# Kernel optimization log

Hardware: AMD Instinct MI355X
Metric: run time of the kernel (lower is better)

Reference implementation:

```python
import jax, jax.numpy as jnp
import numpy as np

U = 1024   # units
DK = 1024  # attention inner dim (dk)
B, T, D = 64, 128, 256


def setup_inputs() -> dict:
    key = jax.random.key(0)
    ks = jax.random.split(key, 20)
    s_w = 0.02   # dense-kernel init scale
    s_a = 0.03   # ~glorot for (1, dk) attention vectors
    inp = {
        'x': jax.random.normal(ks[0], (B, T, D), jnp.float32),
        'kernel': jax.random.normal(ks[1], (D, 5 * U), jnp.float32) * s_w,
        'recurrent_kernel': jax.random.normal(ks[2], (U, 5 * U), jnp.float32) * s_w,
        'cell_kernel': jax.random.normal(ks[3], (U, 5 * U), jnp.float32) * s_w,
        'bias': jnp.zeros((5 * U,), jnp.float32),
        'aggregation': jax.random.normal(ks[4], (3 * U, U), jnp.float32) * s_w,
    }
    att_names = ['up_att_downl', 'up_att_downr', 'up_att_randl', 'up_att_randr',
                 'rand_att_upl', 'rand_att_upr', 'rand_att_downl', 'rand_att_downr',
                 'down_att_upl', 'down_att_upr', 'down_att_randl', 'down_att_randr']
    for i, n in enumerate(att_names):
        inp[n] = jax.random.normal(ks[5 + i], (1, DK), jnp.float32) * s_a
    return inp


def _cumsoftmax_l2r(x):
    return jnp.cumsum(jax.nn.softmax(x, axis=-1), axis=-1)


def _cumsoftmax_r2l(x):
    # reverse, softmax+cumsum, reverse back (softmax is permutation-equivariant)
    return jnp.cumsum(jax.nn.softmax(x, axis=-1)[..., ::-1], axis=-1)[..., ::-1]


def _forward(x, kernel, recurrent_kernel, cell_kernel, bias, aggregation,
             up_att_downl, up_att_downr, up_att_randl, up_att_randr,
             rand_att_upl, rand_att_upr, rand_att_downl, rand_att_downr,
             down_att_upl, down_att_upr, down_att_randl, down_att_randr):
    # Rank-1 collapse of (v w_l)(u w_r)^T v chains: scalar = w_l . w_r
    s_ud = jnp.sum(up_att_downl * up_att_downr)
    s_ur = jnp.sum(up_att_randl * up_att_randr)
    s_ru = jnp.sum(rand_att_upl * rand_att_upr)
    s_rd = jnp.sum(rand_att_downl * rand_att_downr)
    s_du = jnp.sum(down_att_upl * down_att_upr)
    s_dr = jnp.sum(down_att_randl * down_att_randr)

    # precompute input projection for all timesteps: [T, B, 5U]
    xw = jnp.einsum('btd,dk->tbk', x, kernel) + bias

    def step(carry, xw_t):
        c, h = carry
        z = xw_t + h @ recurrent_kernel + c @ cell_kernel  # [B, 5U]
        up = _cumsoftmax_l2r(z[:, :U])
        down = _cumsoftmax_r2l(z[:, U:2 * U])
        rand = z[:, 2 * U:3 * U]
        du = jnp.sum(down * up, axis=-1, keepdims=True)    # <down, up> per batch
        ru = jnp.sum(rand * up, axis=-1, keepdims=True)
        dr = jnp.sum(down * rand, axis=-1, keepdims=True)
        O1 = jax.nn.sigmoid(s_ud * up * du) + jax.nn.sigmoid(s_ur * up * ru)
        O2 = jax.nn.sigmoid(s_ru * rand * ru) + jax.nn.sigmoid(s_rd * rand * dr)
        O3 = jax.nn.sigmoid(s_du * down * du) + jax.nn.sigmoid(s_dr * down * dr)
        f_gate = jax.nn.sigmoid(jnp.concatenate([O1, O2, O3], axis=-1) @ aggregation)
        i_gate = 1.0 - f_gate
        o_gate = z[:, 3 * U:4 * U]          # NOTE: no sigmoid in the original
        c_in = jnp.tanh(z[:, 4 * U:])
        c_new = f_gate * c + i_gate * c_in
        h_new = o_gate * jnp.tanh(c_new)
        return (c_new, h_new), h_new

    init = (jnp.zeros((x.shape[0], U), x.dtype), jnp.zeros((x.shape[0], U), x.dtype))
    _, hs = jax.lax.scan(step, init, xw)
    return jnp.transpose(hs, (1, 0, 2))  # return_sequences=True -> [B, T, U]


def reference(x, kernel, recurrent_kernel, cell_kernel, bias, aggregation,
              up_att_downl, up_att_downr, up_att_randl, up_att_randr,
              rand_att_upl, rand_att_upr, rand_att_downl, rand_att_downr,
              down_att_upl, down_att_upr, down_att_randl, down_att_randr):
    return _forward(x, kernel, recurrent_kernel, cell_kernel, bias, aggregation,
                    up_att_downl, up_att_downr, up_att_randl, up_att_randr,
                    rand_att_upl, rand_att_upr, rand_att_downl, rand_att_downr,
                    down_att_upl, down_att_upr, down_att_randl, down_att_randr)
```

## Files before the change

kernel.cpp:

```cpp
#include <hip/hip_runtime.h>
#include <hip/hip_bf16.h>


typedef short  bf16x8 __attribute__((ext_vector_type(8)));
typedef float  f32x4  __attribute__((ext_vector_type(4)));
typedef _Float16 f16;
typedef _Float16 f16x8 __attribute__((ext_vector_type(8)));
typedef __hip_bfloat16 bf16;
typedef unsigned long long u64;

#define U 1024
#define BATCH 64
#define TSTEPS 128
#define DIM 256
#define N5 5120
#define K2 2048

#define OFF_WRC   0u
#define OFF_KT    20971520u
#define OFF_AGGT  23592960u
#define OFF_XBF   29884416u
#define OFF_ZP    34078720u
#define OFF_ABUF  39321600u
#define OFF_C32   39845888u
#define OFF_OBUF  40108032u
#define OFF_SCAL  40501248u
#define OFF_CTR   40501504u
#define OFF_PB    OFF_KT

#define NBLK_A 160
#define NBLK_B 64
#define NBLK   224
#define FPAD   8

#define KT_OFF 131072

#define MFMA16(a,b,c)  __builtin_amdgcn_mfma_f32_16x16x32_bf16((a),(b),(c),0,0,0)
#define MFMA16H(a,b,c) __builtin_amdgcn_mfma_f32_16x16x32_f16((a),(b),(c),0,0,0)

__global__ __launch_bounds__(256) void k_xconv(const float* __restrict__ in,
                                               f16* __restrict__ o, int n4) {
    const int i = blockIdx.x * 256 + threadIdx.x;
    if (i < n4) {
        const float4 v = ((const float4*)in)[i];
        f16 tmp[4] = {(f16)v.x, (f16)v.y, (f16)v.z, (f16)v.w};
        ((uint2*)o)[i] = *(const uint2*)tmp;
    }
}

__global__ __launch_bounds__(256) void k_transpose_h(const float* __restrict__ in,
                                                     f16* __restrict__ out,
                                                     int C, int out_stride, int out_off) {
    __shared__ f16 tile[64][65];
    const int tc = blockIdx.x * 64, tr = blockIdx.y * 64;
    const int tx = threadIdx.x & 63, ty0 = threadIdx.x >> 6;
#pragma unroll
    for (int i = 0; i < 64; i += 4)
        tile[ty0 + i][tx] = (f16)(in[(tr + ty0 + i) * C + tc + tx]);
    __syncthreads();
#pragma unroll
    for (int i = 0; i < 64; i += 4)
        out[(tc + ty0 + i) * out_stride + out_off + tr + tx] = tile[tx][ty0 + i];
}

__global__ __launch_bounds__(256) void k_transpose_b(const float* __restrict__ in,
                                                     bf16* __restrict__ out,
                                                     int C, int out_stride, int out_off) {
    __shared__ bf16 tile[64][65];
    const int tc = blockIdx.x * 64, tr = blockIdx.y * 64;
    const int tx = threadIdx.x & 63, ty0 = threadIdx.x >> 6;
#pragma unroll
    for (int i = 0; i < 64; i += 4)
        tile[ty0 + i][tx] = __float2bfloat16(in[(tr + ty0 + i) * C + tc + tx]);
    __syncthreads();
#pragma unroll
    for (int i = 0; i < 64; i += 4)
        out[(tc + ty0 + i) * out_stride + out_off + tr + tx] = tile[tx][ty0 + i];
}

struct AttPtrs { const float* p[12]; };

__global__ __launch_bounds__(256) void k_scal(AttPtrs ap, float* __restrict__ scal) {
    __shared__ float red[256];
    const int tid = threadIdx.x;
    for (int q = 0; q < 6; ++q) {
        const float* l = ap.p[2 * q];
        const float* r = ap.p[2 * q + 1];
        float s = 0.f;
        for (int i = tid; i < 1024; i += 256)
            s += l[i] * r[i];
        red[tid] = s; __syncthreads();
        for (int o = 128; o > 0; o >>= 1) {
            if (tid < o) red[tid] += red[tid + o];
            __syncthreads();
        }
        if (tid == 0) scal[q] = red[0];
        __syncthreads();
    }
}

__device__ __forceinline__ float wave_sum(float v) {
#pragma unroll
    for (int o = 32; o > 0; o >>= 1) v += __shfl_xor(v, o, 64);
    return v;
}
__device__ __forceinline__ float wave_max(float v) {
#pragma unroll
    for (int o = 32; o > 0; o >>= 1) v = fmaxf(v, __shfl_xor(v, o, 64));
    return v;
}
__device__ __forceinline__ float wave_scan(float v, int lane) {
#pragma unroll
    for (int o = 1; o < 64; o <<= 1) {
        float n = __shfl_up(v, o, 64);
        if (lane >= o) v += n;
    }
    return v;
}
__device__ __forceinline__ float block_sum(float v, float* sm4, int w, int lane) {
    float s = wave_sum(v);
    if (lane == 0) sm4[w] = s;
    __syncthreads();
    float r = sm4[0] + sm4[1] + sm4[2] + sm4[3];
    __syncthreads();
    return r;
}
__device__ __forceinline__ float block_max(float v, float* sm4, int w, int lane) {
    float s = wave_max(v);
    if (lane == 0) sm4[w] = s;
    __syncthreads();
    float r = fmaxf(fmaxf(sm4[0], sm4[1]), fmaxf(sm4[2], sm4[3]));
    __syncthreads();
    return r;
}
__device__ __forceinline__ float block_scan(float v, float* sm4, int w, int lane, float* total) {
    float ws = wave_scan(v, lane);
    if (lane == 63) sm4[w] = ws;
    __syncthreads();
    float base = 0.f;
    if (w > 0) base += sm4[0];
    if (w > 1) base += sm4[1];
    if (w > 2) base += sm4[2];
    *total = sm4[0] + sm4[1] + sm4[2] + sm4[3];
    __syncthreads();
    return base + ws;
}
__device__ __forceinline__ float sigm(float x) { return 1.f / (1.f + __expf(-x)); }

__device__ __forceinline__ u64 ald64(const void* p) {
    return __hip_atomic_load((const u64*)p, __ATOMIC_RELAXED, __HIP_MEMORY_SCOPE_AGENT);
}
__device__ __forceinline__ bf16x8 ald16B(const bf16* p) {
    union { bf16x8 v; u64 u[2]; } r;
    r.u[0] = ald64(p);
    r.u[1] = ald64((const char*)p + 8);
    return r.v;
}
__device__ __forceinline__ f16x8 aldh16B(const f16* p) {
    union { f16x8 v; u64 u[2]; } r;
    r.u[0] = ald64(p);
    r.u[1] = ald64((const char*)p + 8);
    return r.v;
}
__device__ __forceinline__ f32x4 ald_f4(const float* p) {
    union { f32x4 v; u64 u[2]; } r;
    r.u[0] = ald64(p);
    r.u[1] = ald64(p + 2);
    return r.v;
}
__device__ __forceinline__ float ald_f(const float* p) {
    return __hip_atomic_load(p, __ATOMIC_RELAXED, __HIP_MEMORY_SCOPE_AGENT);
}
__device__ __forceinline__ void ast64(void* p, u64 v) {
    __hip_atomic_store((u64*)p, v, __ATOMIC_RELAXED, __HIP_MEMORY_SCOPE_AGENT);
}
__device__ __forceinline__ void ast32(void* p, unsigned v) {
    __hip_atomic_store((unsigned*)p, v, __ATOMIC_RELAXED, __HIP_MEMORY_SCOPE_AGENT);
}
__device__ __forceinline__ unsigned h16bits(f16 h) {
    unsigned short s; __builtin_memcpy(&s, &h, 2); return (unsigned)s;
}
__device__ __forceinline__ u64 packf2(float a, float b) {
    union { float f[2]; u64 u; } r; r.f[0] = a; r.f[1] = b; return r.u;
}

__device__ __forceinline__ void signal_flag(int* f, int v) {
    __syncthreads();
    if (threadIdx.x == 0)
        __hip_atomic_store(f, v, __ATOMIC_RELAXED, __HIP_MEMORY_SCOPE_AGENT);
}
__device__ __forceinline__ void wait_ge(const int* f, int n, int tgt) {
    if (threadIdx.x < 64) {
        for (;;) {
            int mn = 0x7fffffff;
            for (int i = threadIdx.x; i < n; i += 64) {
                const int v = __hip_atomic_load(f + i * FPAD, __ATOMIC_RELAXED,
                                                __HIP_MEMORY_SCOPE_AGENT);
                mn = v < mn ? v : mn;
            }
            if (__all(mn >= tgt)) break;
            __builtin_amdgcn_s_sleep(1);
        }
    }
    __syncthreads();
}

__device__ __forceinline__ bf16x8 lds_rd(const char* s, int nloc, int kb, int rs) {
    return *(const bf16x8*)(s + nloc * rs + (kb ^ ((nloc & 7) << 4)));
}
__device__ __forceinline__ f16x8 lds_rdh(const char* s, int nloc, int kb, int rs) {
    return *(const f16x8*)(s + nloc * rs + (kb ^ ((nloc & 7) << 4)));
}

__global__ __launch_bounds__(256, 1) void k_persist(
    const f16* __restrict__ xbf, const f16* __restrict__ kt,
    const f16* __restrict__ wrct, const bf16* __restrict__ aggt,
    float* __restrict__ zp, f16* __restrict__ abuf,
    float* __restrict__ c32, bf16* __restrict__ obuf,
    float* __restrict__ pbuf,
    const float* __restrict__ scal, const float* __restrict__ bias,
    float* __restrict__ out, int* __restrict__ ctr)
{
    __shared__ __align__(16) char smem[147456];
    __shared__ float sm4[4];

    const int bid = blockIdx.x, tid = threadIdx.x;
    const int w = tid >> 6, lane = tid & 63;
    const int ml = lane & 15, q = lane >> 4;
    int* fA = ctr;
    int* fB = ctr + 1280;
    int* fC = ctr + 1792;
    int* fP = ctr + 2304;

    if (bid < NBLK_A) {
        const int cg = bid >> 2;
        const int kq = bid & 3;
        const int n0 = cg * 128;
        const int kwbase = (kq < 2) ? kq * 512 : 1024 + (kq - 2) * 512;
        const int kA0 = (kq & 1) * 512;

        for (int i = 0; i < 32; ++i) {
            const int cid = i * 256 + tid;
            const int row = cid >> 6, k = (cid & 63) * 8;
            f16x8 v = *(const f16x8*)(wrct + (size_t)(n0 + row) * K2 + kwbase + k);
            *(f16x8*)(smem + row * 1024 + ((k * 2) ^ ((row & 7) << 4))) = v;
        }
        for (int i = 0; i < 4; ++i) {
            const int cid = i * 256 + tid;
            const int row = cid >> 3, k = (cid & 7) * 8;
            f16x8 v = *(const f16x8*)(kt + (size_t)(n0 + row) * DIM + kq * 64 + k);
            *(f16x8*)(smem + KT_OFF + row * 128 + ((k * 2) ^ ((row & 7) << 4))) = v;
        }
        __syncthreads();

        const int arow = w * 16 + ml;
        const f16* hP = abuf + (kq < 2 ? 0 : 1) * 65536 + arow * U + kA0;
        const f16* xrow = xbf + (size_t)arow * TSTEPS * DIM;
        float* zpq = zp + (size_t)kq * 64 * N5;

#define LOADG(G, B) do { \
            const int b_ = (G) * 64 + q * 8; \
            a0[B] = aldh16B(hP + b_); \
            a1[B] = aldh16B(hP + b_ + 32); \
        } while (0)

        for (int t = 0; t < TSTEPS; ++t) {
            f32x4 acc[8];
#pragma unroll
            for (int i = 0; i < 8; ++i) acc[i] = (f32x4){0.f, 0.f, 0.f, 0.f};

#pragma unroll
            for (int cx = 0; cx < 2; ++cx) {
                const f16x8 ax = *(const f16x8*)(xrow + t * DIM + kq * 64 + cx * 32 + q * 8);
#pragma unroll
                for (int ct = 0; ct < 8; ++ct) {
                    const f16x8 b = lds_rdh(smem + KT_OFF, ct * 16 + ml, cx * 64 + q * 16, 128);
                    acc[ct] = MFMA16H(ax, b, acc[ct]);
                }
            }

            wait_ge(fC, NBLK_B, t);

            {
                f16x8 a0[4], a1[4];
                LOADG(0, 0);
                LOADG(1, 1);
                LOADG(2, 2);
#pragma unroll
                for (int g = 0; g < 8; ++g) {
                    if (g < 5) LOADG(g + 3, (g + 3) & 3);
                    const int B_ = g & 3;
#pragma unroll
                    for (int c = 0; c < 2; ++c) {
                        const f16x8 a = c ? a1[B_] : a0[B_];
#pragma unroll
                        for (int ct = 0; ct < 8; ++ct) {
                            const f16x8 b = lds_rdh(smem, ct * 16 + ml,
                                                    g * 128 + c * 64 + q * 16, 1024);
                            acc[ct] = MFMA16H(a, b, acc[ct]);
                        }
                    }
                }
            }

#pragma unroll
            for (int ct = 0; ct < 8; ++ct)
#pragma unroll
                for (int r = 0; r < 4; ++r) {
                    const float v = acc[ct][r];
                    const float pv = __shfl_xor(v, 1, 64);
                    if (!(ml & 1)) {
                        const int row = w * 16 + q * 4 + r;
                        const int col = n0 + ct * 16 + ml;
                        ast64(&zpq[row * N5 + col], packf2(v, pv));
                    }
                }
            signal_flag(fA + bid * FPAD, t + 1);
        }
#undef LOADG
    } else {
        const int rb = bid - NBLK_A;
        const int cg = rb >> 2;
        const int kq2 = rb & 3;
        const int nst = cg * 64 + kq2 * 16;
        const int KO = kq2 * 768;

        for (int i = 0; i < 24; ++i) {
            const int cid = i * 256 + tid;
            const int nloc = cid / 96, kc = cid - nloc * 96;
            const int k = kc * 8;
            bf16x8 v = *(const bf16x8*)(aggt + (size_t)(cg * 64 + nloc) * 3072 + KO + k);
            *(bf16x8*)(smem + nloc * 1536 + ((k * 2) ^ ((nloc & 7) << 4))) = v;
        }
        __syncthreads();

        const float s_ud = scal[0], s_ur = scal[1], s_ru = scal[2],
                    s_rd = scal[3], s_du = scal[4], s_dr = scal[5];
        const int rowA = w * 16 + ml;
        const bf16* orow = obuf + rowA * 3072 + KO;
        float* cpriv = c32 + rb * 1024;
        float* pmy   = pbuf + (size_t)rb * 4096;

        for (int t = 0; t < TSTEPS; ++t) {
            wait_ge(fA, 96, t + 1);
            {
                f32x4 zu = {0.f,0.f,0.f,0.f}, zd = {0.f,0.f,0.f,0.f}, zn = {0.f,0.f,0.f,0.f};
#pragma unroll
                for (int kqi = 0; kqi < 4; ++kqi) {
                    const float* bp = zp + (size_t)kqi * 64 * N5 + rb * N5;
                    zu += ald_f4(bp + tid * 4);
                    zd += ald_f4(bp + U + tid * 4);
                    zn += ald_f4(bp + 2 * U + tid * 4);
                }
                zu += ((const f32x4*)bias)[tid];
                zd += ((const f32x4*)(bias + U))[tid];
                zn += ((const f32x4*)(bias + 2 * U))[tid];

                float mup = block_max(fmaxf(fmaxf(zu[0], zu[1]), fmaxf(zu[2], zu[3])), sm4, w, lane);
                const float e0 = __expf(zu[0] - mup), e1 = __expf(zu[1] - mup),
                            e2 = __expf(zu[2] - mup), e3 = __expf(zu[3] - mup);
                float totu;
                float inclu = block_scan(e0 + e1 + e2 + e3, sm4, w, lane, &totu);
                const float exclu = inclu - (e0 + e1 + e2 + e3);
                const float inv_u = 1.f / totu;
                const float u0 = (exclu + e0) * inv_u;
                const float u1 = (exclu + e0 + e1) * inv_u;
                const float u2 = (exclu + e0 + e1 + e2) * inv_u;
                const float u3 = (exclu + e0 + e1 + e2 + e3) * inv_u;

                float mdn = block_max(fmaxf(fmaxf(zd[0], zd[1]), fmaxf(zd[2], zd[3])), sm4, w, lane);
                const float f0 = __expf(zd[0] - mdn), f1 = __expf(zd[1] - mdn),
                            f2 = __expf(zd[2] - mdn), f3 = __expf(zd[3] - mdn);
                float totd;
                float incld = block_scan(f0 + f1 + f2 + f3, sm4, w, lane, &totd);
                const float excld = incld - (f0 + f1 + f2 + f3);
                const float inv_d = 1.f / totd;
                const float d0 = (totd - excld) * inv_d;
                const float d1 = (totd - excld - f0) * inv_d;
                const float d2 = (totd - excld - f0 - f1) * inv_d;
                const float d3 = (totd - excld - f0 - f1 - f2) * inv_d;

                const float du = block_sum(d0 * u0 + d1 * u1 + d2 * u2 + d3 * u3, sm4, w, lane);
                const float ru = block_sum(zn[0] * u0 + zn[1] * u1 + zn[2] * u2 + zn[3] * u3, sm4, w, lane);
                const float dr = block_sum(d0 * zn[0] + d1 * zn[1] + d2 * zn[2] + d3 * zn[3], sm4, w, lane);

                bf16* orw = obuf + rb * 3072;
                const int j0 = tid * 4;
                const float uu[4] = {u0, u1, u2, u3};
                const float dd[4] = {d0, d1, d2, d3};
                const float rr[4] = {zn[0], zn[1], zn[2], zn[3]};
                union { bf16 h[4]; u64 u; } p1, p2, p3;
#pragma unroll
                for (int i = 0; i < 4; ++i) {
                    p1.h[i] = __float2bfloat16(sigm(s_ud * uu[i] * du) + sigm(s_ur * uu[i] * ru));
                    p2.h[i] = __float2bfloat16(sigm(s_ru * rr[i] * ru) + sigm(s_rd * rr[i] * dr));
                    p3.h[i] = __float2bfloat16(sigm(s_du * dd[i] * du) + sigm(s_dr * dd[i] * dr));
                }
                ast64(orw + j0,         p1.u);
                ast64(orw + U + j0,     p2.u);
                ast64(orw + 2 * U + j0, p3.u);
            }
            signal_flag(fB + rb * FPAD, t + 1);

            wait_ge(fA + 96 * FPAD, 64, t + 1);
            float z3v[4], z4v[4];
            {
                const int col = nst + ml;
                const int r0 = w * 16 + q * 4;
#pragma unroll
                for (int r = 0; r < 4; ++r) {
                    z3v[r] = bias[3 * U + col];
                    z4v[r] = bias[4 * U + col];
#pragma unroll
                    for (int kqi = 0; kqi < 4; ++kqi) {
                        const float* zr = zp + (size_t)kqi * 64 * N5 + (size_t)(r0 + r) * N5;
                        z3v[r] += ald_f(zr + 3 * U + col);
                        z4v[r] += ald_f(zr + 4 * U + col);
                    }
                }
            }
            wait_ge(fB, NBLK_B, t + 1);
            {
                f32x4 acc[4];
#pragma unroll
                for (int i = 0; i < 4; ++i) acc[i] = (f32x4){0.f, 0.f, 0.f, 0.f};
                bf16x8 ob[3][8];
#pragma unroll
                for (int G = 0; G < 3; ++G)
#pragma unroll
                    for (int j = 0; j < 8; ++j)
                        ob[G][j] = ald16B(orow + (G * 8 + j) * 32 + q * 8);
#pragma unroll
                for (int g = 0; g < 3; ++g)
#pragma unroll
                    for (int j = 0; j < 8; ++j) {
                        const int kc = g * 8 + j;
#pragma unroll
                        for (int ct = 0; ct < 4; ++ct) {
                            const bf16x8 b = lds_rd(smem, ct * 16 + ml, kc * 64 + q * 16, 1536);
                            acc[ct] = MFMA16(ob[g][j], b, acc[ct]);
                        }
                    }
#pragma unroll
                for (int ct = 0; ct < 4; ++ct)
#pragma unroll
                    for (int r = 0; r < 4; ++r) {
                        const float v = acc[ct][r];
                        const float pv = __shfl_xor(v, 1, 64);
                        if (!(ml & 1)) {
                            const int row = w * 16 + q * 4 + r;
                            ast64(&pmy[row * 64 + ct * 16 + ml], packf2(v, pv));
                        }
                    }
            }
            signal_flag(fP + rb * FPAD, t + 1);
            wait_ge(fP + cg * 4 * FPAD, 4, t + 1);
            {
                const int col = nst + ml;
                const int r0 = w * 16 + q * 4;
#pragma unroll
                for (int r = 0; r < 4; ++r) {
                    const int row = r0 + r;
                    float s = 0.f;
#pragma unroll
                    for (int j = 0; j < 4; ++j)
                        s += ald_f(pbuf + (size_t)(cg * 4 + j) * 4096 + row * 64 + kq2 * 16 + ml);
                    const float f = sigm(s);
                    const float cold = cpriv[row * 16 + ml];
                    const float cn = f * cold + (1.f - f) * tanhf(z4v[r]);
                    const float hn = z3v[r] * tanhf(cn);
                    cpriv[row * 16 + ml] = cn;
                    const f16 hhb = (f16)hn;
                    const f16 ccb = (f16)cn;
                    unsigned vh = h16bits(hhb), vc = h16bits(ccb);
                    const unsigned ph = (unsigned)__shfl_xor((int)vh, 1, 64);
                    const unsigned pc = (unsigned)__shfl_xor((int)vc, 1, 64);
                    if (!(ml & 1)) {
                        const int eo = row * U + col;
                        ast32((unsigned*)(abuf + 0 * 65536 + eo), vh | (ph << 16));
                        ast32((unsigned*)(abuf + 1 * 65536 + eo), vc | (pc << 16));
                    }
                    out[((size_t)row * TSTEPS + t) * U + col] = hn;
                }
            }
            signal_flag(fC + rb * FPAD, t + 1);
        }
    }
}

extern "C" void kernel_launch(void* const* d_in, const int* in_sizes, int n_in,
                              void* d_out, int out_size, void* d_ws, size_t ws_size,
                              hipStream_t stream) {
    (void)in_sizes; (void)n_in; (void)out_size; (void)ws_size;
    const float* x    = (const float*)d_in[0];
    const float* Wk   = (const float*)d_in[1];
    const float* Wr   = (const float*)d_in[2];
    const float* Wc   = (const float*)d_in[3];
    const float* bias = (const float*)d_in[4];
    const float* agg  = (const float*)d_in[5];

    char* ws = (char*)d_ws;
    f16*   wrct = (f16*)(ws + OFF_WRC);
    f16*   kt   = (f16*)(ws + OFF_KT);
    bf16*  aggt = (bf16*)(ws + OFF_AGGT);
    f16*   xbf  = (f16*)(ws + OFF_XBF);
    float* zp   = (float*)(ws + OFF_ZP);
    f16*   abuf = (f16*)(ws + OFF_ABUF);
    float* c32  = (float*)(ws + OFF_C32);
    bf16*  obuf = (bf16*)(ws + OFF_OBUF);
    float* pbuf = (float*)(ws + OFF_PB);
    float* scal = (float*)(ws + OFF_SCAL);
    int*   ctr  = (int*)(ws + OFF_CTR);
    float* out  = (float*)d_out;

    hipMemsetAsync(abuf, 0, 2 * 65536 * sizeof(f16), stream);
    hipMemsetAsync(c32, 0, BATCH * U * sizeof(float), stream);
    hipMemsetAsync(ctr, 0, 12288, stream);

    k_xconv<<<(BATCH * TSTEPS * DIM / 4 + 255) / 256, 256, 0, stream>>>(x, xbf, BATCH * TSTEPS * DIM / 4);
    k_transpose_h<<<dim3(5120 / 64, 1024 / 64), 256, 0, stream>>>(Wr, wrct, 5120, 2048, 0);
    k_transpose_h<<<dim3(5120 / 64, 1024 / 64), 256, 0, stream>>>(Wc, wrct, 5120, 2048, 1024);
    k_transpose_h<<<dim3(5120 / 64, 256 / 64),  256, 0, stream>>>(Wk, kt,   5120, 256, 0);
    k_transpose_b<<<dim3(1024 / 64, 3072 / 64), 256, 0, stream>>>(agg, aggt, 1024, 3072, 0);

    AttPtrs ap;
    for (int i = 0; i < 12; ++i) ap.p[i] = (const float*)d_in[6 + i];
    k_scal<<<1, 256, 0, stream>>>(ap, scal);

    k_persist<<<NBLK, 256, 0, stream>>>(xbf, kt, wrct, aggt, zp, abuf, c32,
                                        obuf, pbuf, scal, bias, out, ctr);
}
```

Baseline: 3.385 ms.

## Narrow recurrent flag waits, batch h loads, interleave partials, defer output stores

Each A-block now waits only on the 32 producer flags whose h or c slice it reads, instead of all B-block flags. It hoists the x-projection loads before the wait and issues all 16 h fragment loads at once. The aggregation partials are stored interleaved so the consumer reads them with a single 16-byte load instead of four scalar loads. The global output store is moved after the completion flag so it no longer delays the next step's producers. Together these aim to shorten the per-timestep critical path between cooperating blocks, at the cost of more registers for the 16 h fragments and a reliance on the flag-to-slice mapping being correct.

After: 3.363 ms. Within noise of the previous version (-0.6%).

```diff
diff --git a/kernel.cpp b/kernel.cpp
--- a/kernel.cpp
+++ b/kernel.cpp
@@ -177,6 +177,9 @@
 __device__ __forceinline__ void ast32(void* p, unsigned v) {
     __hip_atomic_store((unsigned*)p, v, __ATOMIC_RELAXED, __HIP_MEMORY_SCOPE_AGENT);
 }
+__device__ __forceinline__ void ast_f(float* p, float v) {
+    __hip_atomic_store(p, v, __ATOMIC_RELAXED, __HIP_MEMORY_SCOPE_AGENT);
+}
 __device__ __forceinline__ unsigned h16bits(f16 h) {
     unsigned short s; __builtin_memcpy(&s, &h, 2); return (unsigned)s;
 }
@@ -257,49 +260,41 @@
         const f16* hP = abuf + (kq < 2 ? 0 : 1) * 65536 + arow * U + kA0;
         const f16* xrow = xbf + (size_t)arow * TSTEPS * DIM;
         float* zpq = zp + (size_t)kq * 64 * N5;
-
-#define LOADG(G, B) do { \
-            const int b_ = (G) * 64 + q * 8; \
-            a0[B] = aldh16B(hP + b_); \
-            a1[B] = aldh16B(hP + b_ + 32); \
-        } while (0)
+        int* fCmy = fC + ((kq & 1) * 32) * FPAD;
 
         for (int t = 0; t < TSTEPS; ++t) {
+            const f16x8 ax0 = *(const f16x8*)(xrow + t * DIM + kq * 64 + q * 8);
+            const f16x8 ax1 = *(const f16x8*)(xrow + t * DIM + kq * 64 + 32 + q * 8);
+
+            wait_ge(fCmy, 32, t);
+
+            f16x8 a[16];
+#pragma unroll
+            for (int i = 0; i < 16; ++i)
+                a[i] = aldh16B(hP + i * 32 + q * 8);
+
             f32x4 acc[8];
 #pragma unroll
             for (int i = 0; i < 8; ++i) acc[i] = (f32x4){0.f, 0.f, 0.f, 0.f};
 
 #pragma unroll
             for (int cx = 0; cx < 2; ++cx) {
-                const f16x8 ax = *(const f16x8*)(xrow + t * DIM + kq * 64 + cx * 32 + q * 8);
+                const f16x8 axv = cx ? ax1 : ax0;
 #pragma unroll
                 for (int ct = 0; ct < 8; ++ct) {
                     const f16x8 b = lds_rdh(smem + KT_OFF, ct * 16 + ml, cx * 64 + q * 16, 128);
-                    acc[ct] = MFMA16H(ax, b, acc[ct]);
-                }
-            }
-
-            wait_ge(fC, NBLK_B, t);
-
-            {
-                f16x8 a0[4], a1[4];
-                LOADG(0, 0);
-                LOADG(1, 1);
-                LOADG(2, 2);
-#pragma unroll
-                for (int g = 0; g < 8; ++g) {
-                    if (g < 5) LOADG(g + 3, (g + 3) & 3);
-                    const int B_ = g & 3;
-#pragma unroll
-                    for (int c = 0; c < 2; ++c) {
-                        const f16x8 a = c ? a1[B_] : a0[B_];
-#pragma unroll
-                        for (int ct = 0; ct < 8; ++ct) {
-                            const f16x8 b = lds_rdh(smem, ct * 16 + ml,
-                                                    g * 128 + c * 64 + q * 16, 1024);
-                            acc[ct] = MFMA16H(a, b, acc[ct]);
-                        }
-                    }
+                    acc[ct] = MFMA16H(axv, b, acc[ct]);
+                }
+            }
+
+#pragma unroll
+            for (int i = 0; i < 16; ++i) {
+                const int g = i >> 1, c = i & 1;
+#pragma unroll
+                for (int ct = 0; ct < 8; ++ct) {
+                    const f16x8 b = lds_rdh(smem, ct * 16 + ml,
+                                            g * 128 + c * 64 + q * 16, 1024);
+                    acc[ct] = MFMA16H(a[i], b, acc[ct]);
                 }
             }
 
@@ -317,7 +312,6 @@
                 }
             signal_flag(fA + bid * FPAD, t + 1);
         }
-#undef LOADG
     } else {
         const int rb = bid - NBLK_A;
         const int cg = rb >> 2;
@@ -339,7 +333,6 @@
         const int rowA = w * 16 + ml;
         const bf16* orow = obuf + rowA * 3072 + KO;
         float* cpriv = c32 + rb * 1024;
-        float* pmy   = pbuf + (size_t)rb * 4096;
 
         for (int t = 0; t < TSTEPS; ++t) {
             wait_ge(fA, 96, t + 1);
@@ -445,31 +438,28 @@
                 for (int ct = 0; ct < 4; ++ct)
 #pragma unroll
                     for (int r = 0; r < 4; ++r) {
-                        const float v = acc[ct][r];
-                        const float pv = __shfl_xor(v, 1, 64);
-                        if (!(ml & 1)) {
-                            const int row = w * 16 + q * 4 + r;
-                            ast64(&pmy[row * 64 + ct * 16 + ml], packf2(v, pv));
-                        }
+                        const int row = w * 16 + q * 4 + r;
+                        ast_f(&pbuf[(((size_t)cg * 64 + row) * 64 + ct * 16 + ml) * 4 + kq2],
+                              acc[ct][r]);
                     }
             }
             signal_flag(fP + rb * FPAD, t + 1);
             wait_ge(fP + cg * 4 * FPAD, 4, t + 1);
+            float hns[4];
             {
                 const int col = nst + ml;
                 const int r0 = w * 16 + q * 4;
 #pragma unroll
                 for (int r = 0; r < 4; ++r) {
                     const int row = r0 + r;
-                    float s = 0.f;
-#pragma unroll
-                    for (int j = 0; j < 4; ++j)
-                        s += ald_f(pbuf + (size_t)(cg * 4 + j) * 4096 + row * 64 + kq2 * 16 + ml);
+                    const f32x4 pj = ald_f4(&pbuf[(((size_t)cg * 64 + row) * 64 + kq2 * 16 + ml) * 4]);
+                    const float s = (pj[0] + pj[1]) + (pj[2] + pj[3]);
                     const float f = sigm(s);
                     const float cold = cpriv[row * 16 + ml];
                     const float cn = f * cold + (1.f - f) * tanhf(z4v[r]);
                     const float hn = z3v[r] * tanhf(cn);
                     cpriv[row * 16 + ml] = cn;
+                    hns[r] = hn;
                     const f16 hhb = (f16)hn;
                     const f16 ccb = (f16)cn;
                     unsigned vh = h16bits(hhb), vc = h16bits(ccb);
@@ -480,10 +470,16 @@
                         ast32((unsigned*)(abuf + 0 * 65536 + eo), vh | (ph << 16));
                         ast32((unsigned*)(abuf + 1 * 65536 + eo), vc | (pc << 16));
                     }
-                    out[((size_t)row * TSTEPS + t) * U + col] = hn;
                 }
             }
             signal_flag(fC + rb * FPAD, t + 1);
+            {
+                const int col = nst + ml;
+                const int r0 = w * 16 + q * 4;
+#pragma unroll
+                for (int r = 0; r < 4; ++r)
+                    out[((size_t)(r0 + r) * TSTEPS + t) * U + col] = hns[r];
+            }
         }
     }
 }
```
